# Kernel optimization log

Hardware: AMD Instinct MI355X
Metric: run time of the kernel (lower is better)

The kernel has to match this reference:

```python
import jax, jax.numpy as jnp
import numpy as np
import math

B, N, H, OUT = 32, 2048, 256, 128
K = 6            # knn_graph k
ALPHA = 0.2      # GCN2Conv alpha (beta=1 since theta/layer are None)
NEG = 0.2        # leaky_relu negative slope in ASAP
EPS = 1e-5       # batchnorm eps
RATIOS = (0.15, 0.25, 0.5)


def _scatter_add(vals, idx, n):
    # vals [B,E] or [B,E,h], idx [B,E] -> [B,n,...]
    b, e = idx.shape
    gi = (idx + jnp.arange(b)[:, None] * n).reshape(-1)
    flat = vals.reshape((b * e,) + vals.shape[2:])
    return jax.ops.segment_sum(flat, gi, num_segments=b * n).reshape((b, n) + vals.shape[2:])


def _scatter_max(vals, idx, n):
    b, e = idx.shape
    gi = (idx + jnp.arange(b)[:, None] * n).reshape(-1)
    flat = vals.reshape((b * e,) + vals.shape[2:])
    return jax.ops.segment_max(flat, gi, num_segments=b * n).reshape((b, n) + vals.shape[2:])


def _gather(x, idx):
    # x [B,n,...] or [B,n], idx [B,E]
    if x.ndim == 3:
        return jnp.take_along_axis(x, idx[..., None], axis=1)
    return jnp.take_along_axis(x, idx, axis=1)


def _knn_undirected(pos):
    # knn_graph(pos, k=6, loop=True) then to_undirected (coalesced via `valid` mask)
    b, n, _ = pos.shape
    d2 = jnp.sum((pos[:, :, None, :] - pos[:, None, :, :]) ** 2, axis=-1)  # [B,n,n]
    _, nbr = jax.lax.top_k(-d2, K)                # self included (dist 0)
    ctr = jnp.broadcast_to(jnp.arange(n)[None, :, None], (b, n, K)).reshape(b, n * K)
    nbr = nbr.reshape(b, n * K)
    src = jnp.concatenate([nbr, ctr], axis=1)     # symmetrize
    dst = jnp.concatenate([ctr, nbr], axis=1)
    key = src * n + dst
    order = jnp.argsort(key, axis=1)
    src = jnp.take_along_axis(src, order, axis=1)
    dst = jnp.take_along_axis(dst, order, axis=1)
    key = jnp.take_along_axis(key, order, axis=1)
    valid = jnp.concatenate([jnp.ones((b, 1), bool), key[:, 1:] != key[:, :-1]], axis=1)
    return src, dst, valid


def _edge_mlp(pos, src, dst, valid, W1, b1, g, be, m, v, W2, b2):
    # relu(MLP([1,32,1])(||p_i - p_j||)); BN in eval mode; self loops replaced by 1
    d = jnp.linalg.norm(_gather(pos, src) - _gather(pos, dst), axis=-1)  # [B,E]
    t = d[..., None] @ W1 + b1                       # [B,E,32]
    t = (t - m) * jax.lax.rsqrt(v + EPS) * g + be
    t = jax.nn.relu(t)
    w = jax.nn.relu((t @ W2 + b2)[..., 0])
    w = jnp.where(src == dst, 1.0, w)                # add_remaining_self_loops fill=1
    return jnp.where(valid, w, 0.0)                  # coalesce duplicate edges


def _gcn2(x, x0, src, dst, w, Wc):
    # GCN2Conv with beta=1, shared weights: ((1-a)*A_hat x + a*x0) @ W
    n = x.shape[1]
    deg = _scatter_add(w, dst, n)
    dis = jax.lax.rsqrt(jnp.maximum(deg, 1e-12))     # deg >= 1 (self loops)
    norm = _gather(dis, src) * w * _gather(dis, dst)
    agg = _scatter_add(norm[..., None] * _gather(x, src), dst, n)
    return ((1.0 - ALPHA) * agg + ALPHA * x0) @ Wc


def _asap(x, src, dst, valid, w, kpool, Wrel, brel, Wroot, Wlin, blin, Watt, batt,
          lW1, lb1, lW2, lW3, lb3):
    n = x.shape[1]
    # gnn_intra_cluster: GraphConv (add aggregation)
    x_pool = _scatter_add(w[..., None] * _gather(x, src), dst, n) @ Wrel + brel + x @ Wroot
    mj = _gather(x_pool, src)                                    # [B,E,H]
    x_q = _scatter_max(jnp.where(valid[..., None], mj, -jnp.inf), dst, n) @ Wlin + blin
    score = (jnp.concatenate([_gather(x_q, dst), mj], axis=-1) @ Watt + batt)[..., 0]
    score = jnp.where(valid, jax.nn.leaky_relu(score, NEG), -jnp.inf)
    smax = _scatter_max(score, dst, n)
    e = jnp.where(valid, jnp.exp(score - _gather(smax, dst)), 0.0)
    att = e / _gather(_scatter_add(e, dst, n), dst)
    xn = _scatter_add(att[..., None] * _gather(x, src), dst, n)
    # LEConv fitness (no edge weights; duplicates masked)
    a = (xn @ lW1 + lb1)[..., 0]
    bb = (xn @ lW2)[..., 0]
    msg = jnp.where(valid, _gather(a, src) - _gather(bb, dst), 0.0)
    fit = jax.nn.sigmoid(_scatter_add(msg, dst, n) + (xn @ lW3 + lb3)[..., 0])
    vals, idx = jax.lax.top_k(fit, kpool)
    return _gather(xn, idx) * vals[..., None], idx


def _forward(x, pos, conv_W, eW1, eb1, ebn_g, ebn_b, ebn_m, ebn_v, eW2, eb2,
             aWrel, abrel, aWroot, aWlin, ablin, aWatt, abatt,
             leW1, leb1, leW2, leW3, leb3, gW, gb, nW, nb):
    h = None
    readouts = []
    for s in range(4):
        src, dst, valid = _knn_undirected(pos)
        w = _edge_mlp(pos, src, dst, valid, eW1[s], eb1[s], ebn_g[s], ebn_b[s],
                      ebn_m[s], ebn_v[s], eW2[s], eb2[s])
        if s in (1, 2):
            readouts.append(jnp.concatenate([jnp.mean(h, axis=1), jnp.max(h, axis=1)], axis=-1))
        hin = x if s == 0 else h
        h = jax.nn.relu(_gcn2(hin, x, src, dst, w, conv_W[s]))
        if s < 3:
            kpool = math.ceil(RATIOS[s] * h.shape[1])
            h, idx = _asap(h, src, dst, valid, w, kpool, aWrel[s], abrel[s], aWroot[s],
                           aWlin[s], ablin[s], aWatt[s], abatt[s],
                           leW1[s], leb1[s], leW2[s], leW3[s], leb3[s])
            x = _gather(x, idx)
            pos = _gather(pos, idx)
    gate = jax.nn.softmax(h @ gW + gb, axis=1)      # attentional aggregation
    gp = jnp.sum(gate * (h @ nW + nb), axis=1)      # [B,OUT]
    return jnp.concatenate([gp, readouts[1], readouts[0]], axis=-1)


def setup_inputs() -> dict:
    key = jax.random.key(0)
    ks = iter(jax.random.split(key, 40))
    def rn(shape, scale=1.0):
        return scale * jax.random.normal(next(ks), shape, dtype=jnp.float32)
    return {
        "x": rn((B, N, H)),
        "pos": rn((B, N, 3)),
        "conv_W": rn((4, H, H), H ** -0.5),
        "eW1": rn((4, 1, 32)),
        "eb1": rn((4, 32), 0.1),
        "ebn_g": 1.0 + rn((4, 32), 0.1),
        "ebn_b": rn((4, 32), 0.1),
        "ebn_m": rn((4, 32), 0.1),
        "ebn_v": jnp.ones((4, 32), jnp.float32),
        "eW2": rn((4, 32, 1), 32 ** -0.5),
        "eb2": rn((4, 1), 0.1),
        "aWrel": rn((3, H, H), H ** -0.5),
        "abrel": rn((3, H), 0.1),
        "aWroot": rn((3, H, H), H ** -0.5),
        "aWlin": rn((3, H, H), H ** -0.5),
        "ablin": rn((3, H), 0.1),
        "aWatt": rn((3, 2 * H, 1), (2 * H) ** -0.5),
        "abatt": rn((3, 1), 0.1),
        "leW1": rn((3, H, 1), H ** -0.5),
        "leb1": rn((3, 1), 0.1),
        "leW2": rn((3, H, 1), H ** -0.5),
        "leW3": rn((3, H, 1), H ** -0.5),
        "leb3": rn((3, 1), 0.1),
        "gW": rn((H, 1), H ** -0.5),
        "gb": rn((1,), 0.1),
        "nW": rn((H, OUT), H ** -0.5),
        "nb": rn((OUT,), 0.1),
    }


def reference(x, pos, conv_W, eW1, eb1, ebn_g, ebn_b, ebn_m, ebn_v, eW2, eb2,
              aWrel, abrel, aWroot, aWlin, ablin, aWatt, abatt,
              leW1, leb1, leW2, leW3, leb3, gW, gb, nW, nb):
    return _forward(x, pos, conv_W, eW1, eb1, ebn_g, ebn_b, ebn_m, ebn_v, eW2, eb2,
                    aWrel, abrel, aWroot, aWlin, ablin, aWatt, abatt,
                    leW1, leb1, leW2, leW3, leb3, gW, gb, nW, nb)
```

## Files before the change

kernel.cpp:

```cpp
#include <hip/hip_runtime.h>
#include <hip/hip_bf16.h>
#include <math.h>

#define BB 32
#define NMAX 2048
#define HD 256
#define KNN 6
#define OUTD 128
#define NCH 8

typedef __hip_bfloat16 bf16;

__device__ __forceinline__ void xcd_map(int g, int wave, int n, int& b, int& d){
  int P=(n+3)>>2;
  int r=g&7, q=g>>3;
  b=r+8*(q/P);
  d=(q%P)*4+wave;
}

__global__ void k_detect(const void* __restrict__ x, int* __restrict__ flag){
  __shared__ int cnt_s;
  if (threadIdx.x==0) cnt_s=0;
  __syncthreads();
  const unsigned short* u=(const unsigned short*)x;
  int c=0;
  for (int i=threadIdx.x;i<4096;i+=256){
    int e=(u[i]>>7)&0xFF;
    if (e>=0xC0) c++;
  }
  atomicAdd(&cnt_s,c);
  __syncthreads();
  if (threadIdx.x==0) flag[0]=(cnt_s>32)?1:0;
}

__device__ __forceinline__ float loadx(const void* x, int fl, size_t idx){
  if (fl) return ((const float*)x)[idx];
  unsigned short u=((const unsigned short*)x)[idx];
  return __uint_as_float(((unsigned)u)<<16);
}
__device__ __forceinline__ float4 loadx4(const void* x, int fl, size_t idx){
  if (fl) return *(const float4*)((const float*)x+idx);
  float4 r;
  r.x=loadx(x,0,idx); r.y=loadx(x,0,idx+1); r.z=loadx(x,0,idx+2); r.w=loadx(x,0,idx+3);
  return r;
}

__global__ void k_cvtpos(const void* __restrict__ pos, const int* __restrict__ flag,
                         float* __restrict__ posF){
  int t=blockIdx.x*256+threadIdx.x;
  if (t>=BB*NMAX*3) return;
  posF[t]=loadx(pos,flag[0],t);
}
struct WTab { const void* src[25]; int cnt[25]; int dst[25]; };
__global__ void k_cvtw(WTab tab, const int* __restrict__ flag, float* __restrict__ wsW){
  int seg=blockIdx.y;
  int t=blockIdx.x*256+threadIdx.x;
  if (t>=tab.cnt[seg]) return;
  wsW[tab.dst[seg]+t]=loadx(tab.src[seg],flag[0],t);
}

__global__ void k_initcum(int* __restrict__ cum){
  int t=blockIdx.x*256+threadIdx.x;
  if (t<BB*NMAX) cum[t]=t%NMAX;
}
__global__ void k_zero2(int* __restrict__ a, int* __restrict__ b, int n){
  int t=blockIdx.x*256+threadIdx.x;
  if (t<n){ a[t]=0; b[t]=0; }
}
__global__ void k_gatherpos(const float* __restrict__ posF, const int* __restrict__ cum,
                            float* __restrict__ posf, int n){
  int t=blockIdx.x*256+threadIdx.x;
  if (t>=BB*n*3) return;
  int c=t%3, i=(t/3)%n, b=t/(3*n);
  posf[t]=posF[((size_t)b*NMAX+cum[b*NMAX+i])*3+c];
}

__global__ void k_knn_part(const float* __restrict__ posf, double* __restrict__ dcand,
                           int* __restrict__ icand, int n){
  int b=blockIdx.z, ch=blockIdx.y;
  int i=blockIdx.x*256+threadIdx.x;
  const float* pp=posf+(size_t)b*n*3;
  int cs=(n+NCH-1)/NCH;
  int jlo=ch*cs, jhi=jlo+cs; if (jhi>n) jhi=n;
  float pxf=0.f,pyf=0.f,pzf=0.f;
  double px=0.0,py=0.0,pz=0.0;
  if (i<n){
    pxf=pp[i*3]; pyf=pp[i*3+1]; pzf=pp[i*3+2];
    px=(double)pxf; py=(double)pyf; pz=(double)pzf;
  }
  double bd0=INFINITY,bd1=INFINITY,bd2=INFINITY,bd3=INFINITY,bd4=INFINITY,bd5=INFINITY;
  float bd5f=INFINITY;
  int   bi0=0x7fffffff,bi1=0x7fffffff,bi2=0x7fffffff,bi3=0x7fffffff,bi4=0x7fffffff,bi5=0x7fffffff;
  __shared__ float sx[256],sy[256],sz[256];
  for (int base=jlo;base<jhi;base+=256){
    int j=base+threadIdx.x;
    if (j<jhi){ sx[threadIdx.x]=pp[j*3]; sy[threadIdx.x]=pp[j*3+1]; sz[threadIdx.x]=pp[j*3+2]; }
    __syncthreads();
    int lim=jhi-base; if (lim>256) lim=256;
    if (i<n){
      for (int t=0;t<lim;t++){
        float dxf=pxf-sx[t], dyf=pyf-sy[t], dzf=pzf-sz[t];
        float d2f=fmaf(dxf,dxf,fmaf(dyf,dyf,dzf*dzf));
        if (d2f<=bd5f){
          double dx=__dsub_rn(px,(double)sx[t]);
          double dy=__dsub_rn(py,(double)sy[t]);
          double dz=__dsub_rn(pz,(double)sz[t]);
          double d2=__dadd_rn(__dadd_rn(__dmul_rn(dx,dx),__dmul_rn(dy,dy)),__dmul_rn(dz,dz));
          if (d2<bd5){
            int id=base+t;
            if (d2<bd4){ bd5=bd4; bi5=bi4;
              if (d2<bd3){ bd4=bd3; bi4=bi3;
                if (d2<bd2){ bd3=bd2; bi3=bi2;
                  if (d2<bd1){ bd2=bd1; bi2=bi1;
                    if (d2<bd0){ bd1=bd0; bi1=bi0; bd0=d2; bi0=id; }
                    else { bd1=d2; bi1=id; }
                  } else { bd2=d2; bi2=id; }
                } else { bd3=d2; bi3=id; }
              } else { bd4=d2; bi4=id; }
            } else { bd5=d2; bi5=id; }
            bd5f=(float)(bd5*1.00001);
          }
        }
      }
    }
    __syncthreads();
  }
  if (i<n){
    size_t o=(((size_t)b*NCH+ch)*n+i)*KNN;
    dcand[o+0]=bd0; dcand[o+1]=bd1; dcand[o+2]=bd2; dcand[o+3]=bd3; dcand[o+4]=bd4; dcand[o+5]=bd5;
    icand[o+0]=bi0; icand[o+1]=bi1; icand[o+2]=bi2; icand[o+3]=bi3; icand[o+4]=bi4; icand[o+5]=bi5;
  }
}

__global__ void k_knn_merge(const double* __restrict__ dcand, const int* __restrict__ icand,
                            int* __restrict__ nbr, int n){
  int t=blockIdx.x*256+threadIdx.x;
  if (t>=BB*n) return;
  int b=t/n, i=t-b*n;
  double cd[NCH*KNN]; int ci[NCH*KNN];
  #pragma unroll
  for (int ch=0;ch<NCH;ch++){
    size_t o=(((size_t)b*NCH+ch)*n+i)*KNN;
    #pragma unroll
    for (int k=0;k<KNN;k++){ cd[ch*KNN+k]=dcand[o+k]; ci[ch*KNN+k]=icand[o+k]; }
  }
  int* out=nbr+(size_t)t*KNN;
  #pragma unroll
  for (int k=0;k<KNN;k++){
    int best=0;
    for (int q=1;q<NCH*KNN;q++){
      bool lt=(cd[q]<cd[best])||(cd[q]==cd[best]&&ci[q]<ci[best]);
      if (lt) best=q;
    }
    out[k]=ci[best];
    cd[best]=INFINITY; ci[best]=0x7fffffff;
  }
}

__global__ void k_edge(const float* __restrict__ posf, const int* __restrict__ nbr,
                       float* __restrict__ w1, float* __restrict__ w2,
                       unsigned char* __restrict__ val2, int* __restrict__ cnt,
                       const float* __restrict__ W1, const float* __restrict__ b1,
                       const float* __restrict__ g,  const float* __restrict__ be,
                       const float* __restrict__ m,  const float* __restrict__ v,
                       const float* __restrict__ W2, const float* __restrict__ b2p,
                       int n){
  int t=blockIdx.x*256+threadIdx.x;
  if (t>=BB*n*KNN) return;
  int k=t%KNN; int c=(t/KNN)%n; int b=t/(KNN*n);
  const int* nb=nbr+(size_t)b*n*KNN;
  int j=nb[c*KNN+k];
  atomicAdd(&cnt[b*n+j],1);
  bool dup=false;
  #pragma unroll
  for (int kk=0;kk<KNN;kk++) dup=dup||(nb[j*KNN+kk]==c);
  const float* pp=posf+(size_t)b*n*3;
  double dx=__dsub_rn((double)pp[c*3+0],(double)pp[j*3+0]);
  double dy=__dsub_rn((double)pp[c*3+1],(double)pp[j*3+1]);
  double dz=__dsub_rn((double)pp[c*3+2],(double)pp[j*3+2]);
  double d2=__dadd_rn(__dadd_rn(__dmul_rn(dx,dx),__dmul_rn(dy,dy)),__dmul_rn(dz,dz));
  float dd=(float)sqrt(d2);
  float wv;
  if (j==c) wv=1.0f;
  else {
    float acc=b2p[0];
    for (int q=0;q<32;q++){
      float tt=dd*W1[q]+b1[q];
      float r=1.0f/sqrtf(v[q]+1e-5f);
      tt=(tt-m[q])*r*g[q]+be[q];
      tt=fmaxf(tt,0.f);
      acc=fmaf(tt,W2[q],acc);
    }
    wv=fmaxf(acc,0.f);
  }
  w1[t]=wv;
  w2[t]=dup?0.f:wv;
  val2[t]=dup?0:1;
}

__global__ void k_csr_scan(const int* __restrict__ cnt, int* __restrict__ offs, int n){
  int b=blockIdx.x, t=threadIdx.x;
  int L=(n+255)/256;
  __shared__ int ssum[256];
  int lo=t*L, hi=lo+L; if (hi>n) hi=n; if (lo>n) lo=n;
  int s=0;
  for (int i=lo;i<hi;i++) s+=cnt[b*n+i];
  ssum[t]=s;
  __syncthreads();
  if (t==0){
    int run=0;
    for (int q=0;q<256;q++){ int vv=ssum[q]; ssum[q]=run; run+=vv; }
  }
  __syncthreads();
  int run=ssum[t];
  for (int i=lo;i<hi;i++){ offs[b*(n+1)+i]=run; run+=cnt[b*n+i]; }
  if (lo<n && hi==n) offs[b*(n+1)+n]=run;
}
__global__ void k_csr_fill(const int* __restrict__ nbr, const int* __restrict__ offs,
                           int* __restrict__ cur, int* __restrict__ rev, int n){
  int t=blockIdx.x*256+threadIdx.x;
  if (t>=BB*n*KNN) return;
  int b=t/(n*KNN); int rem=t-b*n*KNN;
  int d=nbr[t];
  int slot=offs[b*(n+1)+d]+atomicAdd(&cur[b*n+d],1);
  if (slot<0) slot=0;
  if (slot>=n*KNN) slot=n*KNN-1;
  rev[(size_t)b*n*KNN+slot]=rem;
}
__global__ void k_sortdeg(int* __restrict__ rev, const int* __restrict__ offs,
                          const float* __restrict__ w1, const float* __restrict__ w2,
                          float* __restrict__ dis, int n){
  int t=blockIdx.x*256+threadIdx.x;
  if (t>=BB*n) return;
  int b=t/n, d=t-b*n;
  size_t base=(size_t)b*n*KNN;
  int lo=offs[b*(n+1)+d], hi=offs[b*(n+1)+d+1];
  for (int a2=lo+1;a2<hi;a2++){
    int vv=rev[base+a2]; int p=a2;
    while (p>lo && rev[base+p-1]>vv){ rev[base+p]=rev[base+p-1]; p--; }
    rev[base+p]=vv;
  }
  float s=0.f;
  #pragma unroll
  for (int k=0;k<KNN;k++) s+=w1[(size_t)t*KNN+k];
  for (int sl=lo;sl<hi;sl++) s+=w2[base+rev[base+sl]];
  dis[t]=1.0f/sqrtf(fmaxf(s,1e-12f));
}

template<int MODE,int RAW>
__global__ void k_nbrsum(const float* __restrict__ Hin, const float* __restrict__ w1,
                         const float* __restrict__ w2, const int* __restrict__ nbr,
                         const int* __restrict__ rev, const int* __restrict__ offs,
                         const float* __restrict__ dis, const void* __restrict__ xraw,
                         const int* __restrict__ flag,
                         const int* __restrict__ cum, float* __restrict__ outp, int n){
  int b,d;
  xcd_map(blockIdx.x,threadIdx.x>>6,n,b,d);
  int lane=threadIdx.x&63;
  if (d>=n) return;
  int wid=b*n+d;
  int fl=flag[0];
  const float* Hb=Hin+(size_t)b*n*HD;
  float4 a=make_float4(0.f,0.f,0.f,0.f);
  float dd=(MODE==0)?dis[wid]:0.f;
  int c4=lane*4;
  #pragma unroll
  for (int k=0;k<KNN;k++){
    int sN=nbr[(size_t)wid*KNN+k];
    float wv=w1[(size_t)wid*KNN+k];
    float nm=(MODE==0)?dis[b*n+sN]*wv*dd:wv;
    float4 r = RAW ? loadx4(xraw,fl,((size_t)b*n+sN)*HD+c4)
                   : *(const float4*)(Hb+(size_t)sN*HD+c4);
    a.x=fmaf(nm,r.x,a.x); a.y=fmaf(nm,r.y,a.y); a.z=fmaf(nm,r.z,a.z); a.w=fmaf(nm,r.w,a.w);
  }
  size_t rbase=(size_t)b*n*KNN;
  int lo=offs[b*(n+1)+d], hi=offs[b*(n+1)+d+1];
  for (int sl=lo;sl<hi;sl++){
    int e=rev[rbase+sl];
    int sN=e/KNN;
    float wv=w2[rbase+e];
    float nm=(MODE==0)?dis[b*n+sN]*wv*dd:wv;
    float4 r = RAW ? loadx4(xraw,fl,((size_t)b*n+sN)*HD+c4)
                   : *(const float4*)(Hb+(size_t)sN*HD+c4);
    a.x=fmaf(nm,r.x,a.x); a.y=fmaf(nm,r.y,a.y); a.z=fmaf(nm,r.z,a.z); a.w=fmaf(nm,r.w,a.w);
  }
  if (MODE==0){
    float4 xr=loadx4(xraw,fl,((size_t)b*NMAX+cum[b*NMAX+d])*HD+c4);
    a.x=0.8f*a.x+0.2f*xr.x; a.y=0.8f*a.y+0.2f*xr.y;
    a.z=0.8f*a.z+0.2f*xr.z; a.w=0.8f*a.w+0.2f*xr.w;
  }
  *(float4*)(outp+(size_t)wid*HD+c4)=a;
}

__global__ void k_mm(const float* __restrict__ A1, const float* __restrict__ B1,
                     const float* __restrict__ A2, const float* __restrict__ B2,
                     const float* __restrict__ bias, int relu,
                     float* __restrict__ Cout, int M){
  __shared__ __align__(16) float As[16][68];
  __shared__ __align__(16) float Bs[16][260];
  int tid=threadIdx.x, bm=blockIdx.x;
  int tr=tid>>5, tc=tid&31;
  float acc[8][8];
  #pragma unroll
  for (int i=0;i<8;i++){
    #pragma unroll
    for (int j=0;j<8;j++) acc[i][j]=0.f;
  }
  int l=tid*4;
  int ar=l>>4, ak=l&15;
  int arow=bm*64+ar;
  int KT = A2 ? 512 : 256;
  for (int k0=0;k0<KT;k0+=16){
    const float* Asrc=(k0<HD)?A1:A2;
    const float* Bsrc=(k0<HD)?B1:B2;
    int kc=k0&(HD-1);
    if (arow<M){
      float4 a4=*(const float4*)(Asrc+(size_t)arow*HD+kc+ak);
      As[ak][ar]=a4.x; As[ak+1][ar]=a4.y; As[ak+2][ar]=a4.z; As[ak+3][ar]=a4.w;
    } else {
      As[ak][ar]=0.f; As[ak+1][ar]=0.f; As[ak+2][ar]=0.f; As[ak+3][ar]=0.f;
    }
    #pragma unroll
    for (int c=0;c<4;c++){
      int idx=c*256+tid;
      int rkk=idx>>6, cc=(idx&63)*4;
      *(float4*)&Bs[rkk][cc]=*(const float4*)(Bsrc+(size_t)(kc+rkk)*HD+cc);
    }
    __syncthreads();
    #pragma unroll
    for (int kk=0;kk<16;kk++){
      float af[8], bf[8];
      *(float4*)&af[0]=*(const float4*)&As[kk][tr*8];
      *(float4*)&af[4]=*(const float4*)&As[kk][tr*8+4];
      *(float4*)&bf[0]=*(const float4*)&Bs[kk][tc*8];
      *(float4*)&bf[4]=*(const float4*)&Bs[kk][tc*8+4];
      #pragma unroll
      for (int i=0;i<8;i++){
        #pragma unroll
        for (int j=0;j<8;j++) acc[i][j]=fmaf(af[i],bf[j],acc[i][j]);
      }
    }
    __syncthreads();
  }
  #pragma unroll
  for (int i=0;i<8;i++){
    int grow=bm*64+tr*8+i;
    if (grow>=M) continue;
    #pragma unroll
    for (int j=0;j<8;j++){
      int gcol=tc*8+j;
      float v=acc[i][j];
      if (bias) v+=bias[gcol];
      if (relu) v=fmaxf(v,0.f);
      Cout[(size_t)grow*HD+gcol]=v;
    }
  }
}

__global__ void k_va(const float* __restrict__ Wlin, const float* __restrict__ wa,
                     const float* __restrict__ blin, float* __restrict__ va){
  int i=threadIdx.x;
  float acc=0.f;
  for (int j=0;j<HD;j++) acc=fmaf(Wlin[(size_t)i*HD+j],wa[j],acc);
  va[i]=acc;
  if (i==0){
    float c=0.f;
    for (int j=0;j<HD;j++) c=fmaf(blin[j],wa[j],c);
    va[256]=c;
  }
}

__global__ void k_qd(const float* __restrict__ T, const float* __restrict__ wb,
                     const float* __restrict__ va, const int* __restrict__ nbr,
                     const int* __restrict__ rev, const int* __restrict__ offs,
                     const unsigned char* __restrict__ val2,
                     float* __restrict__ pb, float* __restrict__ qd, int n){
  int b,d;
  xcd_map(blockIdx.x,threadIdx.x>>6,n,b,d);
  int lane=threadIdx.x&63;
  if (d>=n) return;
  int wid=b*n+d;
  int c4=lane*4;
  float4 r1=*(const float4*)(T+(size_t)wid*HD+c4);
  float4 wb4=*(const float4*)(wb+c4);
  float p=r1.x*wb4.x+r1.y*wb4.y+r1.z*wb4.z+r1.w*wb4.w;
  const float* Tb=T+(size_t)b*n*HD;
  float4 m4=make_float4(-INFINITY,-INFINITY,-INFINITY,-INFINITY);
  #pragma unroll
  for (int k=0;k<KNN;k++){
    int sN=nbr[(size_t)wid*KNN+k];
    float4 r=*(const float4*)(Tb+(size_t)sN*HD+c4);
    m4.x=fmaxf(m4.x,r.x); m4.y=fmaxf(m4.y,r.y); m4.z=fmaxf(m4.z,r.z); m4.w=fmaxf(m4.w,r.w);
  }
  size_t rbase=(size_t)b*n*KNN;
  int lo=offs[b*(n+1)+d], hi=offs[b*(n+1)+d+1];
  for (int sl=lo;sl<hi;sl++){
    int e=rev[rbase+sl];
    if (!val2[rbase+e]) continue;
    int sN=e/KNN;
    float4 r=*(const float4*)(Tb+(size_t)sN*HD+c4);
    m4.x=fmaxf(m4.x,r.x); m4.y=fmaxf(m4.y,r.y); m4.z=fmaxf(m4.z,r.z); m4.w=fmaxf(m4.w,r.w);
  }
  float4 va4=*(const float4*)(va+c4);
  float q=va4.x*m4.x+va4.y*m4.y+va4.z*m4.z+va4.w*m4.w;
  #pragma unroll
  for (int o=32;o>0;o>>=1){ p+=__shfl_xor(p,o); q+=__shfl_xor(q,o); }
  if (lane==0){ pb[wid]=p; qd[wid]=q+va[256]; }
}

__global__ void k_attxn(const float* __restrict__ Hin, const float* __restrict__ pb,
                        const float* __restrict__ qd, const int* __restrict__ nbr,
                        const int* __restrict__ rev, const int* __restrict__ offs,
                        const unsigned char* __restrict__ val2, const float* __restrict__ abatt,
                        const float* __restrict__ lW1, const float* __restrict__ lb1,
                        const float* __restrict__ lW2, const float* __restrict__ lW3,
                        const float* __restrict__ lb3,
                        float* __restrict__ av, float* __restrict__ bbv, float* __restrict__ l3v,
                        float* __restrict__ Tout, int n){
  int b,d;
  xcd_map(blockIdx.x,threadIdx.x>>6,n,b,d);
  int lane=threadIdx.x&63;
  if (d>=n) return;
  int wid=b*n+d;
  float batt=abatt[0];
  float qs=qd[wid];
  const float* Hb=Hin+(size_t)b*n*HD;
  int c4=lane*4;
  size_t rbase=(size_t)b*n*KNN;
  int lo=offs[b*(n+1)+d], hi=offs[b*(n+1)+d+1];
  float smax=-INFINITY;
  #pragma unroll
  for (int k=0;k<KNN;k++){
    int sN=nbr[(size_t)wid*KNN+k];
    float sc=qs+pb[b*n+sN]+batt;
    sc=sc>=0.f?sc:0.2f*sc;
    smax=fmaxf(smax,sc);
  }
  for (int sl=lo;sl<hi;sl++){
    int e=rev[rbase+sl];
    if (!val2[rbase+e]) continue;
    int sN=e/KNN;
    float sc=qs+pb[b*n+sN]+batt;
    sc=sc>=0.f?sc:0.2f*sc;
    smax=fmaxf(smax,sc);
  }
  float es=0.f;
  float4 a=make_float4(0.f,0.f,0.f,0.f);
  #pragma unroll
  for (int k=0;k<KNN;k++){
    int sN=nbr[(size_t)wid*KNN+k];
    float sc=qs+pb[b*n+sN]+batt;
    sc=sc>=0.f?sc:0.2f*sc;
    float e2=expf(sc-smax);
    es+=e2;
    float4 r=*(const float4*)(Hb+(size_t)sN*HD+c4);
    a.x=fmaf(e2,r.x,a.x); a.y=fmaf(e2,r.y,a.y); a.z=fmaf(e2,r.z,a.z); a.w=fmaf(e2,r.w,a.w);
  }
  for (int sl=lo;sl<hi;sl++){
    int e=rev[rbase+sl];
    if (!val2[rbase+e]) continue;
    int sN=e/KNN;
    float sc=qs+pb[b*n+sN]+batt;
    sc=sc>=0.f?sc:0.2f*sc;
    float e2=expf(sc-smax);
    es+=e2;
    float4 r=*(const float4*)(Hb+(size_t)sN*HD+c4);
    a.x=fmaf(e2,r.x,a.x); a.y=fmaf(e2,r.y,a.y); a.z=fmaf(e2,r.z,a.z); a.w=fmaf(e2,r.w,a.w);
  }
  float inv=1.f/es;
  a.x*=inv; a.y*=inv; a.z*=inv; a.w*=inv;
  *(float4*)(Tout+(size_t)wid*HD+c4)=a;
  float4 w1v=*(const float4*)(lW1+c4);
  float4 w2v=*(const float4*)(lW2+c4);
  float4 w3v=*(const float4*)(lW3+c4);
  float s1=a.x*w1v.x+a.y*w1v.y+a.z*w1v.z+a.w*w1v.w;
  float s2=a.x*w2v.x+a.y*w2v.y+a.z*w2v.z+a.w*w2v.w;
  float s3=a.x*w3v.x+a.y*w3v.y+a.z*w3v.z+a.w*w3v.w;
  #pragma unroll
  for (int o=32;o>0;o>>=1){ s1+=__shfl_xor(s1,o); s2+=__shfl_xor(s2,o); s3+=__shfl_xor(s3,o); }
  if (lane==0){ av[wid]=s1+lb1[0]; bbv[wid]=s2; l3v[wid]=s3+lb3[0]; }
}

__global__ void k_fit(const float* __restrict__ av, const float* __restrict__ bbv,
                      const float* __restrict__ l3v, const int* __restrict__ nbr,
                      const int* __restrict__ rev, const int* __restrict__ offs,
                      const unsigned char* __restrict__ val2, float* __restrict__ fit, int n){
  int t=blockIdx.x*256+threadIdx.x;
  if (t>=BB*n) return;
  int b=t/n, d=t-b*n;
  size_t rbase=(size_t)b*n*KNN;
  float ms=0.f; int cv=KNN;
  #pragma unroll
  for (int k=0;k<KNN;k++) ms+=av[b*n+nbr[(size_t)t*KNN+k]];
  int lo=offs[b*(n+1)+d], hi=offs[b*(n+1)+d+1];
  for (int sl=lo;sl<hi;sl++){
    int e=rev[rbase+sl];
    if (val2[rbase+e]){ ms+=av[b*n+e/KNN]; cv++; }
  }
  float z=ms-(float)cv*bbv[t]+l3v[t];
  fit[t]=1.f/(1.f+expf(-z));
}

__global__ void k_rank(const float* __restrict__ fit, float* __restrict__ svl,
                       int* __restrict__ sid, int n, int kp){
  __shared__ float sf[2048];
  int b=blockIdx.y;
  int i=blockIdx.x*256+threadIdx.x;
  const float* fb=fit+(size_t)b*n;
  for (int j=threadIdx.x;j<n;j+=256) sf[j]=fb[j];
  __syncthreads();
  if (i>=n) return;
  float fi=sf[i];
  int rank=0;
  for (int j=0;j<n;j++){
    float fj=sf[j];
    if (fj>fi || (fj==fi && j<i)) rank++;
  }
  if (rank<kp){ svl[b*NMAX+rank]=fi; sid[b*NMAX+rank]=i; }
}

__global__ void k_pool(const float* __restrict__ T, const float* __restrict__ svl,
                       const int* __restrict__ sid, const int* __restrict__ cumA,
                       int* __restrict__ cumB, float* __restrict__ Hout, int n, int kp){
  int wid=blockIdx.x*4+(threadIdx.x>>6);
  int lane=threadIdx.x&63;
  if (wid>=BB*kp) return;
  int b=wid/kp, j=wid-b*kp;
  int srcn=sid[b*NMAX+j];
  if (srcn<0) srcn=0;
  if (srcn>=n) srcn=n-1;
  float vv=svl[b*NMAX+j];
  int c4=lane*4;
  float4 r=*(const float4*)(T+((size_t)b*n+srcn)*HD+c4);
  r.x*=vv; r.y*=vv; r.z*=vv; r.w*=vv;
  *(float4*)(Hout+((size_t)b*kp+j)*HD+c4)=r;
  if (lane==0) cumB[b*NMAX+j]=cumA[b*NMAX+srcn];
}

__global__ void k_readout(const float* __restrict__ Hb, float* __restrict__ ro, int n){
  int b=blockIdx.x, h=threadIdx.x;
  const float* p=Hb+(size_t)b*n*HD+h;
  float s=0.f, m=-INFINITY;
  for (int i=0;i<n;i++){ float v=p[(size_t)i*HD]; s+=v; m=fmaxf(m,v); }
  ro[b*512+h]=s/(float)n;
  ro[b*512+256+h]=m;
}

__global__ void k_final(const float* __restrict__ Hb, const float* __restrict__ gW,
                        const float* __restrict__ gb, const float* __restrict__ nW,
                        const float* __restrict__ nbias, const float* __restrict__ ro0,
                        const float* __restrict__ ro1, float* __restrict__ outp, int n){
  int b=blockIdx.x, tid=threadIdx.x;
  int wv=tid>>6, lane=tid&63;
  __shared__ float gate[64];
  for (int i=wv;i<n;i+=4){
    const float* r=Hb+((size_t)b*n+i)*HD;
    float p=0.f;
    for (int h=lane;h<HD;h+=64) p=fmaf(r[h],gW[h],p);
    #pragma unroll
    for (int o=32;o>0;o>>=1) p+=__shfl_xor(p,o);
    if (lane==0) gate[i]=p+gb[0];
  }
  __syncthreads();
  if (tid==0){
    float mx=-INFINITY;
    for (int i=0;i<n;i++) mx=fmaxf(mx,gate[i]);
    float sm=0.f;
    for (int i=0;i<n;i++){ gate[i]=expf(gate[i]-mx); sm+=gate[i]; }
    float inv=1.f/sm;
    for (int i=0;i<n;i++) gate[i]*=inv;
  }
  __syncthreads();
  if (tid<OUTD){
    float acc=0.f;
    for (int i=0;i<n;i++){
      const float* r=Hb+((size_t)b*n+i)*HD;
      float dot=0.f;
      for (int h=0;h<HD;h++) dot=fmaf(r[h],nW[(size_t)h*OUTD+tid],dot);
      acc=fmaf(gate[i],dot+nbias[tid],acc);
    }
    outp[(size_t)b*1152+tid]=acc;
  }
  for (int q=tid;q<512;q+=256){
    outp[(size_t)b*1152+128+q]=ro1[b*512+q];
    outp[(size_t)b*1152+640+q]=ro0[b*512+q];
  }
}

extern "C" void kernel_launch(void* const* d_in, const int* in_sizes, int n_in,
                              void* d_out, int out_size, void* d_ws, size_t ws_size,
                              hipStream_t stream){
  if (n_in<27) return;
  if (in_sizes[0]!=BB*NMAX*HD || in_sizes[1]!=BB*NMAX*3) return;
  float* outp=(float*)d_out;
  (void)out_size;

  char* p=(char*)d_ws;
  auto carve=[&](size_t bytes)->char*{ char* r=p; p+=((bytes+255)/256)*256; return r; };
  float* posF=(float*)carve((size_t)BB*NMAX*3*4);
  float* posf=(float*)carve((size_t)BB*NMAX*3*4);
  float* Hbuf=(float*)carve((size_t)BB*NMAX*HD*4);
  float* Tbuf=(float*)carve((size_t)BB*NMAX*HD*4);
  static const int wcnt[25]={262144,128,128,128,128,128,128,128,4,
                             196608,768,196608,196608,768,1536,3,
                             768,3,768,768,3,256,1,32768,128};
  int woff[25]; int wtot=0;
  for (int i=0;i<25;i++){ woff[i]=wtot; wtot+=(wcnt[i]+63)&~63; }
  float* wsW=(float*)carve((size_t)wtot*4);
  int*   nbr =(int*)  carve((size_t)BB*NMAX*KNN*4);
  int*   rev =(int*)  carve((size_t)BB*NMAX*KNN*4);
  float* w1  =(float*)carve((size_t)BB*NMAX*KNN*4);
  float* w2  =(float*)carve((size_t)BB*NMAX*KNN*4);
  unsigned char* val2=(unsigned char*)carve((size_t)BB*NMAX*KNN);
  int* cnt  =(int*)carve((size_t)BB*NMAX*4);
  int* offs =(int*)carve((size_t)BB*(NMAX+1)*4);
  int* cur  =(int*)carve((size_t)BB*NMAX*4);
  float* dis=(float*)carve((size_t)BB*NMAX*4);
  float* pb =(float*)carve((size_t)BB*NMAX*4);
  float* qd =(float*)carve((size_t)BB*NMAX*4);
  float* av =(float*)carve((size_t)BB*NMAX*4);
  float* bbv=(float*)carve((size_t)BB*NMAX*4);
  float* l3v=(float*)carve((size_t)BB*NMAX*4);
  float* fit=(float*)carve((size_t)BB*NMAX*4);
  float* svl=(float*)carve((size_t)BB*NMAX*4);
  int*   sid=(int*)  carve((size_t)BB*NMAX*4);
  int* cumA =(int*)carve((size_t)BB*NMAX*4);
  int* cumB =(int*)carve((size_t)BB*NMAX*4);
  int* flag =(int*)carve(256);
  float* va =(float*)carve(272*4);
  float* ro0=(float*)carve((size_t)BB*512*4);
  float* ro1=(float*)carve((size_t)BB*512*4);
  size_t need=(size_t)(p-(char*)d_ws);
  if (ws_size<need) return;

  double* dcand=(double*)Tbuf;
  int*    icand=(int*)((char*)Tbuf + (size_t)BB*NCH*NMAX*KNN*8);

  k_detect<<<1,256,0,stream>>>(d_in[0],flag);
  k_cvtpos<<<(BB*NMAX*3+255)/256,256,0,stream>>>(d_in[1],flag,posF);
  {
    WTab tab;
    int maxc=0;
    for (int i=0;i<25;i++){ tab.src[i]=d_in[2+i]; tab.cnt[i]=wcnt[i]; tab.dst[i]=woff[i]; if (wcnt[i]>maxc) maxc=wcnt[i]; }
    k_cvtw<<<dim3((maxc+255)/256,25),256,0,stream>>>(tab,flag,wsW);
  }
  k_initcum<<<(BB*NMAX+255)/256,256,0,stream>>>(cumA);

  const int NS[4]={2048,308,77,39};
  const int KP[3]={308,77,39};

  for (int s=0;s<4;s++){
    int n=NS[s]; int M=BB*n;
    int gG=BB*((n+3)/4);
    const float* wconv =wsW+woff[0]+(size_t)s*65536;
    const float* eW1p  =wsW+woff[1]+s*32;
    const float* eb1p  =wsW+woff[2]+s*32;
    const float* gp    =wsW+woff[3]+s*32;
    const float* bep   =wsW+woff[4]+s*32;
    const float* mp    =wsW+woff[5]+s*32;
    const float* vp    =wsW+woff[6]+s*32;
    const float* W2p   =wsW+woff[7]+s*32;
    const float* b2p   =wsW+woff[8]+s;
    const float* aWrelp=wsW+woff[9]+(size_t)s*65536;
    const float* abrelp=wsW+woff[10]+s*256;
    const float* aWrootp=wsW+woff[11]+(size_t)s*65536;
    const float* aWlinp=wsW+woff[12]+(size_t)s*65536;
    const float* ablinp=wsW+woff[13]+s*256;
    const float* wap   =wsW+woff[14]+s*512;
    const float* wbp   =wsW+woff[14]+s*512+256;
    const float* abattp=wsW+woff[15]+s;
    const float* leW1p =wsW+woff[16]+s*256;
    const float* leb1p =wsW+woff[17]+s;
    const float* leW2p =wsW+woff[18]+s*256;
    const float* leW3p =wsW+woff[19]+s*256;
    const float* leb3p =wsW+woff[20]+s;

    const float* pf;
    if (s==0){
      pf=posF;
    } else {
      k_gatherpos<<<(BB*n*3+255)/256,256,0,stream>>>(posF,cumA,posf,n);
      pf=posf;
    }
    k_knn_part<<<dim3((n+255)/256,NCH,BB),256,0,stream>>>(pf,dcand,icand,n);
    k_knn_merge<<<(BB*n+255)/256,256,0,stream>>>(dcand,icand,nbr,n);
    int totE=BB*n*KNN;
    k_zero2<<<(BB*n+255)/256,256,0,stream>>>(cnt,cur,BB*n);
    k_edge<<<(totE+255)/256,256,0,stream>>>(pf,nbr,w1,w2,val2,cnt,
        eW1p,eb1p,gp,bep,mp,vp,W2p,b2p,n);
    k_csr_scan<<<BB,256,0,stream>>>(cnt,offs,n);
    k_csr_fill<<<(totE+255)/256,256,0,stream>>>(nbr,offs,cur,rev,n);
    k_sortdeg<<<(BB*n+255)/256,256,0,stream>>>(rev,offs,w1,w2,dis,n);
    if (s==1) k_readout<<<BB,256,0,stream>>>(Hbuf,ro0,n);
    if (s==2) k_readout<<<BB,256,0,stream>>>(Hbuf,ro1,n);
    if (s==0)
      k_nbrsum<0,1><<<gG,256,0,stream>>>(nullptr,w1,w2,nbr,rev,offs,dis,d_in[0],flag,cumA,Tbuf,n);
    else
      k_nbrsum<0,0><<<gG,256,0,stream>>>(Hbuf,w1,w2,nbr,rev,offs,dis,d_in[0],flag,cumA,Tbuf,n);
    k_mm<<<(M+63)/64,256,0,stream>>>(Tbuf,wconv,(const float*)nullptr,(const float*)nullptr,
                                     (const float*)nullptr,1,Hbuf,M);
    if (s<3){
      int kp=KP[s];
      k_nbrsum<1,0><<<gG,256,0,stream>>>(Hbuf,w1,w2,nbr,rev,offs,dis,d_in[0],flag,cumA,Tbuf,n);
      k_mm<<<(M+63)/64,256,0,stream>>>(Tbuf,aWrelp,Hbuf,aWrootp,abrelp,0,Tbuf,M);
      k_va<<<1,256,0,stream>>>(aWlinp,wap,ablinp,va);
      k_qd<<<gG,256,0,stream>>>(Tbuf,wbp,va,nbr,rev,offs,val2,pb,qd,n);
      k_attxn<<<gG,256,0,stream>>>(Hbuf,pb,qd,nbr,rev,offs,val2,abattp,
                                   leW1p,leb1p,leW2p,leW3p,leb3p,av,bbv,l3v,Tbuf,n);
      k_fit<<<(BB*n+255)/256,256,0,stream>>>(av,bbv,l3v,nbr,rev,offs,val2,fit,n);
      k_rank<<<dim3((n+255)/256,BB),256,0,stream>>>(fit,svl,sid,n,kp);
      k_pool<<<(BB*kp+3)/4,256,0,stream>>>(Tbuf,svl,sid,cumA,cumB,Hbuf,n,kp);
      { int* t=cumA; cumA=cumB; cumB=t; }
    }
  }
  k_final<<<BB,256,0,stream>>>(Hbuf,wsW+woff[21],wsW+woff[22],wsW+woff[23],wsW+woff[24],
                               ro0,ro1,outp,NS[3]);
}
```

Measured before the change: 2.102 ms.

## Prefetch GEMM tiles into registers, fuse counter zeroing, vectorize readout

Three changes. The k_mm GEMM now loads the next K-slice of A and B into registers while the current slice is computed from shared memory, and it gets launch bounds of 256 threads with 4 blocks per CU. The separate zeroing kernel is folded into k_knn_merge, which removes one launch per stage. k_readout now has four waves each read float4 rows in parallel and then combine their partial sums and maxes in shared memory, replacing one thread per column walking every row serially. The prefetch raises register pressure, and the launch-bounds limit could force spills.

```diff
diff --git a/kernel.cpp b/kernel.cpp
--- a/kernel.cpp
+++ b/kernel.cpp
@@ -62,10 +62,6 @@
 __global__ void k_initcum(int* __restrict__ cum){
   int t=blockIdx.x*256+threadIdx.x;
   if (t<BB*NMAX) cum[t]=t%NMAX;
-}
-__global__ void k_zero2(int* __restrict__ a, int* __restrict__ b, int n){
-  int t=blockIdx.x*256+threadIdx.x;
-  if (t<n){ a[t]=0; b[t]=0; }
 }
 __global__ void k_gatherpos(const float* __restrict__ posF, const int* __restrict__ cum,
                             float* __restrict__ posf, int n){
@@ -133,9 +129,11 @@
 }
 
 __global__ void k_knn_merge(const double* __restrict__ dcand, const int* __restrict__ icand,
-                            int* __restrict__ nbr, int n){
+                            int* __restrict__ nbr, int* __restrict__ cnt, int* __restrict__ cur,
+                            int n){
   int t=blockIdx.x*256+threadIdx.x;
   if (t>=BB*n) return;
+  cnt[t]=0; cur[t]=0;
   int b=t/n, i=t-b*n;
   double cd[NCH*KNN]; int ci[NCH*KNN];
   #pragma unroll
@@ -292,10 +290,11 @@
   *(float4*)(outp+(size_t)wid*HD+c4)=a;
 }
 
-__global__ void k_mm(const float* __restrict__ A1, const float* __restrict__ B1,
-                     const float* __restrict__ A2, const float* __restrict__ B2,
-                     const float* __restrict__ bias, int relu,
-                     float* __restrict__ Cout, int M){
+__global__ __launch_bounds__(256,4)
+void k_mm(const float* __restrict__ A1, const float* __restrict__ B1,
+          const float* __restrict__ A2, const float* __restrict__ B2,
+          const float* __restrict__ bias, int relu,
+          float* __restrict__ Cout, int M){
   __shared__ __align__(16) float As[16][68];
   __shared__ __align__(16) float Bs[16][260];
   int tid=threadIdx.x, bm=blockIdx.x;
@@ -309,24 +308,28 @@
   int l=tid*4;
   int ar=l>>4, ak=l&15;
   int arow=bm*64+ar;
+  int brow[4], bcol[4];
+  #pragma unroll
+  for (int c=0;c<4;c++){ int idx=c*256+tid; brow[c]=idx>>6; bcol[c]=(idx&63)*4; }
   int KT = A2 ? 512 : 256;
+  float4 a4; float4 b4[4];
+  a4 = (arow<M)? *(const float4*)(A1+(size_t)arow*HD+ak) : make_float4(0.f,0.f,0.f,0.f);
+  #pragma unroll
+  for (int c=0;c<4;c++) b4[c]=*(const float4*)(B1+(size_t)brow[c]*HD+bcol[c]);
   for (int k0=0;k0<KT;k0+=16){
-    const float* Asrc=(k0<HD)?A1:A2;
-    const float* Bsrc=(k0<HD)?B1:B2;
-    int kc=k0&(HD-1);
-    if (arow<M){
-      float4 a4=*(const float4*)(Asrc+(size_t)arow*HD+kc+ak);
-      As[ak][ar]=a4.x; As[ak+1][ar]=a4.y; As[ak+2][ar]=a4.z; As[ak+3][ar]=a4.w;
-    } else {
-      As[ak][ar]=0.f; As[ak+1][ar]=0.f; As[ak+2][ar]=0.f; As[ak+3][ar]=0.f;
-    }
+    As[ak][ar]=a4.x; As[ak+1][ar]=a4.y; As[ak+2][ar]=a4.z; As[ak+3][ar]=a4.w;
     #pragma unroll
-    for (int c=0;c<4;c++){
-      int idx=c*256+tid;
-      int rkk=idx>>6, cc=(idx&63)*4;
-      *(float4*)&Bs[rkk][cc]=*(const float4*)(Bsrc+(size_t)(kc+rkk)*HD+cc);
-    }
+    for (int c=0;c<4;c++) *(float4*)&Bs[brow[c]][bcol[c]]=b4[c];
     __syncthreads();
+    int k1=k0+16;
+    if (k1<KT){
+      const float* Asrc=(k1<HD)?A1:A2;
+      const float* Bsrc=(k1<HD)?B1:B2;
+      int kc=k1&(HD-1);
+      a4 = (arow<M)? *(const float4*)(Asrc+(size_t)arow*HD+kc+ak) : make_float4(0.f,0.f,0.f,0.f);
+      #pragma unroll
+      for (int c=0;c<4;c++) b4[c]=*(const float4*)(Bsrc+(size_t)(kc+brow[c])*HD+bcol[c]);
+    }
     #pragma unroll
     for (int kk=0;kk<16;kk++){
       float af[8], bf[8];
@@ -538,12 +541,25 @@
 }
 
 __global__ void k_readout(const float* __restrict__ Hb, float* __restrict__ ro, int n){
-  int b=blockIdx.x, h=threadIdx.x;
-  const float* p=Hb+(size_t)b*n*HD+h;
-  float s=0.f, m=-INFINITY;
-  for (int i=0;i<n;i++){ float v=p[(size_t)i*HD]; s+=v; m=fmaxf(m,v); }
-  ro[b*512+h]=s/(float)n;
-  ro[b*512+256+h]=m;
+  __shared__ float ss[4][256], sm[4][256];
+  int b=blockIdx.x, tid=threadIdx.x;
+  int wv=tid>>6, lane=tid&63;
+  int c4=lane*4;
+  float4 s=make_float4(0.f,0.f,0.f,0.f);
+  float4 m=make_float4(-INFINITY,-INFINITY,-INFINITY,-INFINITY);
+  for (int i=wv;i<n;i+=4){
+    float4 v=*(const float4*)(Hb+((size_t)b*n+i)*HD+c4);
+    s.x+=v.x; s.y+=v.y; s.z+=v.z; s.w+=v.w;
+    m.x=fmaxf(m.x,v.x); m.y=fmaxf(m.y,v.y); m.z=fmaxf(m.z,v.z); m.w=fmaxf(m.w,v.w);
+  }
+  *(float4*)&ss[wv][c4]=s;
+  *(float4*)&sm[wv][c4]=m;
+  __syncthreads();
+  int h=tid;
+  float acc=ss[0][h]+ss[1][h]+ss[2][h]+ss[3][h];
+  float mx=fmaxf(fmaxf(sm[0][h],sm[1][h]),fmaxf(sm[2][h],sm[3][h]));
+  ro[b*512+h]=acc/(float)n;
+  ro[b*512+256+h]=mx;
 }
 
 __global__ void k_final(const float* __restrict__ Hb, const float* __restrict__ gW,
@@ -683,9 +699,8 @@
       pf=posf;
     }
     k_knn_part<<<dim3((n+255)/256,NCH,BB),256,0,stream>>>(pf,dcand,icand,n);
-    k_knn_merge<<<(BB*n+255)/256,256,0,stream>>>(dcand,icand,nbr,n);
+    k_knn_merge<<<(BB*n+255)/256,256,0,stream>>>(dcand,icand,nbr,cnt,cur,n);
     int totE=BB*n*KNN;
-    k_zero2<<<(BB*n+255)/256,256,0,stream>>>(cnt,cur,BB*n);
     k_edge<<<(totE+255)/256,256,0,stream>>>(pf,nbr,w1,w2,val2,cnt,
         eW1p,eb1p,gp,bep,mp,vp,W2p,b2p,n);
     k_csr_scan<<<BB,256,0,stream>>>(cnt,offs,n);
```

After: 2.282 ms. 1.09x slower.
